# Kernel tuning notes

Measured on AMD Instinct MI355X. Metric: run time of the kernel, lower is better.

## Reference

```python
import jax, jax.numpy as jnp
import numpy as np

D_MODEL = 1024
NUM_HEADS = 16
D_K = D_MODEL // NUM_HEADS


def setup_inputs() -> dict:
    key = jax.random.key(0)
    ks = jax.random.split(key, 5)
    s = 1.0 / np.sqrt(D_MODEL)
    return {
        "x": jax.random.normal(ks[0], (2, 2048, D_MODEL), dtype=jnp.float32),
        "Wq": jax.random.normal(ks[1], (D_MODEL, D_MODEL), dtype=jnp.float32) * s,
        "bq": jnp.zeros((D_MODEL,), dtype=jnp.float32),
        "Wk": jax.random.normal(ks[2], (D_MODEL, D_MODEL), dtype=jnp.float32) * s,
        "bk": jnp.zeros((D_MODEL,), dtype=jnp.float32),
        "Wv": jax.random.normal(ks[3], (D_MODEL, D_MODEL), dtype=jnp.float32) * s,
        "bv": jnp.zeros((D_MODEL,), dtype=jnp.float32),
        "Wo": jax.random.normal(ks[4], (D_MODEL, D_MODEL), dtype=jnp.float32) * s,
        "bo": jnp.zeros((D_MODEL,), dtype=jnp.float32),
    }


def reference(x, Wq, bq, Wk, bk, Wv, bv, Wo, bo):
    B, S, D = x.shape
    H, dk = NUM_HEADS, D_K
    Q = x @ Wq + bq  # [B, S, D]
    K = x @ Wk + bk
    V = x @ Wv + bv
    # Faithful to the torch code: plain .view(B, H, S, dk) (NO transpose),
    # i.e. heads are carved out of the flattened (S*D) dim, not the feature dim.
    Q = Q.reshape(B, H, S, dk)
    K = K.reshape(B, H, S, dk)
    V = V.reshape(B, H, S, dk)
    scores = jnp.einsum("bhqd,bhkd->bhqk", Q, K) / jnp.sqrt(jnp.float32(dk))
    attn = jax.nn.softmax(scores, axis=-1)  # [B, H, S, S]
    ctx = jnp.einsum("bhqk,bhkd->bhqd", attn, V)  # [B, H, S, dk]
    out = ctx.reshape(B, S, D) @ Wo + bo
    return out  # dropout is identity in eval mode
```

## Files before the change

### kernel.cpp

```cpp
#include <hip/hip_runtime.h>
#include <hip/hip_bf16.h>
#include <math.h>

#define D_MODEL 1024
#define SEQ     2048
#define BATCH   2
#define NHEAD   16
#define DKH     64
#define BH      (BATCH * NHEAD)

typedef unsigned short u16;
typedef unsigned int   u32;
typedef __bf16 bf16x8 __attribute__((ext_vector_type(8)));
typedef float  f32x4  __attribute__((ext_vector_type(4)));

#define MFMA16(a, b, c) __builtin_amdgcn_mfma_f32_16x16x32_bf16((a), (b), (c), 0, 0, 0)
#define AS1 __attribute__((address_space(1)))
#define AS3 __attribute__((address_space(3)))

#define QSCALE 0.18033688f

__device__ __forceinline__ u16 f2bf(float x) {
    u32 u = __float_as_uint(x);
    u += 0x7fffu + ((u >> 16) & 1u);
    return (u16)(u >> 16);
}
__device__ __forceinline__ float bf2f(u16 b) {
    return __uint_as_float(((u32)b) << 16);
}
__device__ __forceinline__ void gl16(const u16* g, void* lds) {
    __builtin_amdgcn_global_load_lds((const AS1 u32*)g, (AS3 u32*)lds, 16, 0, 0);
}

__global__ __launch_bounds__(256) void conv_all(
    const float* __restrict__ x, u16* __restrict__ Xh, int n4,
    const float* __restrict__ W0, const float* __restrict__ W1,
    const float* __restrict__ W2, const float* __restrict__ W3,
    u16* __restrict__ H0, u16* __restrict__ L0, u16* __restrict__ H1, u16* __restrict__ L1,
    u16* __restrict__ H2, u16* __restrict__ L2, u16* __restrict__ H3, u16* __restrict__ L3)
{
    const int t = threadIdx.x;
    if ((int)blockIdx.x < 4096) {
        int i = blockIdx.x * 256 + t;
        if (i >= n4) return;
        float4 v = reinterpret_cast<const float4*>(x)[i];
        uint2 H;
        H.x = f2bf(v.x) | ((u32)f2bf(v.y) << 16);
        H.y = f2bf(v.z) | ((u32)f2bf(v.w) << 16);
        reinterpret_cast<uint2*>(Xh)[i] = H;
        return;
    }
    int id = blockIdx.x - 4096;
    int bx = id & 15, by = (id >> 4) & 15, bz = id >> 8;
    const float* W; u16 *Ht, *Lt;
    if (bz == 0)      { W = W0; Ht = H0; Lt = L0; }
    else if (bz == 1) { W = W1; Ht = H1; Lt = L1; }
    else if (bz == 2) { W = W2; Ht = H2; Lt = L2; }
    else              { W = W3; Ht = H3; Lt = L3; }

    __shared__ float T[64][65];
    const int n0 = bx * 64, k0 = by * 64;
    #pragma unroll
    for (int i = 0; i < 4; ++i) {
        int f = t + i * 256;
        int kr = f >> 4, ns = (f & 15) * 4;
        float4 v = *reinterpret_cast<const float4*>(&W[(size_t)(k0 + kr) * D_MODEL + n0 + ns]);
        T[kr][ns + 0] = v.x; T[kr][ns + 1] = v.y; T[kr][ns + 2] = v.z; T[kr][ns + 3] = v.w;
    }
    __syncthreads();
    #pragma unroll
    for (int i = 0; i < 4; ++i) {
        int f = t + i * 256;
        int nr = f >> 4, ks = (f & 15) * 4;
        u16 hh[4], ll[4];
        #pragma unroll
        for (int j = 0; j < 4; ++j) {
            float xv = T[ks + j][nr];
            u16 hb = f2bf(xv);
            hh[j] = hb;
            ll[j] = f2bf(xv - bf2f(hb));
        }
        uint2 H, L;
        H.x = hh[0] | ((u32)hh[1] << 16); H.y = hh[2] | ((u32)hh[3] << 16);
        L.x = ll[0] | ((u32)ll[1] << 16); L.y = ll[2] | ((u32)ll[3] << 16);
        size_t o = (size_t)(n0 + nr) * D_MODEL + k0 + ks;
        *reinterpret_cast<uint2*>(&Ht[o]) = H;
        *reinterpret_cast<uint2*>(&Lt[o]) = L;
    }
}

__global__ __launch_bounds__(512, 2) void gemm_qkv(
    const u16* __restrict__ AhG,
    const u16* __restrict__ Bqh, const u16* __restrict__ Bql,
    const u16* __restrict__ Bkh, const u16* __restrict__ Bkl,
    const u16* __restrict__ Bvh, const u16* __restrict__ Bvl,
    const float* __restrict__ bq, const float* __restrict__ bk, const float* __restrict__ bv,
    u16* __restrict__ Qb, u16* __restrict__ Kb, u16* __restrict__ Vb)
{
    constexpr int K = D_MODEL, N = D_MODEL;
    __shared__ u16 LB[2][28672];

    const int tid  = threadIdx.x;
    const int wv   = tid >> 6;
    const int lane = tid & 63;
    const int quad = lane >> 4;
    const int l16  = lane & 15;
    const int wm   = wv & 1, wn = wv >> 1;
    const int brow = blockIdx.y * 128, bcol = blockIdx.x * 128;

    const u16* sp[7];
    int sldb[7];
    #pragma unroll
    for (int j = 0; j < 7; ++j) {
        int c = (j < 3) ? (wv * 3 + j)
              : (j < 5) ? (24 + wv * 2 + (j - 3))
                        : (40 + wv * 2 + (j - 5));
        int a = c >> 3, cc = c & 7;
        int row = cc * 16 + (lane >> 2);
        int gseg = (lane & 3) ^ ((lane >> 3) & 3);
        const u16* p;
        if (a == 0)      p = AhG;
        else if (a == 1) p = Bqh;
        else if (a == 2) p = Bql;
        else if (a == 3) p = Bkh;
        else if (a == 4) p = Bkl;
        else if (a == 5) p = Bvh;
        else             p = Bvl;
        int rbase = (a == 0) ? brow : bcol;
        sp[j]   = p + (size_t)(rbase + row) * K + gseg * 8;
        sldb[j] = a * 8192 + cc * 1024;
    }

    int aro[4], bro[2];
    #pragma unroll
    for (int i = 0; i < 4; ++i) {
        int mr = wm * 64 + i * 16 + l16;
        aro[i] = mr * 64 + ((quad ^ ((mr >> 1) & 3)) * 16);
    }
    #pragma unroll
    for (int i = 0; i < 2; ++i) {
        int nr = wn * 32 + i * 16 + l16;
        bro[i] = nr * 64 + ((quad ^ ((nr >> 1) & 3)) * 16);
    }

    f32x4 acc[3][4][2] = {};

    auto rdB = [&](int cur, int m, bf16x8 (&bh)[2], bf16x8 (&bl)[2]) {
        const int bbh = (1 + 2 * m) * 8192, bbl = (2 + 2 * m) * 8192;
        #pragma unroll
        for (int i = 0; i < 2; ++i) {
            bh[i] = *reinterpret_cast<const bf16x8*>((const char*)LB[cur] + bbh + bro[i]);
            bl[i] = *reinterpret_cast<const bf16x8*>((const char*)LB[cur] + bbl + bro[i]);
        }
    };
    auto mm = [&](int m, bf16x8 (&ah)[4], bf16x8 (&bh)[2], bf16x8 (&bl)[2]) {
        __builtin_amdgcn_s_setprio(1);
        #pragma unroll
        for (int mi = 0; mi < 4; ++mi)
            #pragma unroll
            for (int ni = 0; ni < 2; ++ni) {
                f32x4 c = acc[m][mi][ni];
                c = MFMA16(ah[mi], bh[ni], c);
                c = MFMA16(ah[mi], bl[ni], c);
                acc[m][mi][ni] = c;
            }
        __builtin_amdgcn_s_setprio(0);
    };

    #pragma unroll
    for (int j = 0; j < 7; ++j)
        gl16(sp[j], (char*)LB[0] + sldb[j]);

    for (int it = 0; it < K / 32 - 1; ++it) {
        const int cur = it & 1, nx = cur ^ 1;
        const int k1 = (it + 1) * 32;
        bf16x8 ah[4], bh[2], bl[2];

        asm volatile("s_waitcnt vmcnt(4)" ::: "memory");
        __builtin_amdgcn_s_barrier();
        #pragma unroll
        for (int i = 0; i < 4; ++i)
            ah[i] = *reinterpret_cast<const bf16x8*>((const char*)LB[cur] + aro[i]);
        rdB(cur, 0, bh, bl);
        gl16(sp[0] + k1, (char*)LB[nx] + sldb[0]);
        gl16(sp[1] + k1, (char*)LB[nx] + sldb[1]);
        gl16(sp[2] + k1, (char*)LB[nx] + sldb[2]);
        mm(0, ah, bh, bl);

        asm volatile("s_waitcnt vmcnt(5)" ::: "memory");
        __builtin_amdgcn_s_barrier();
        rdB(cur, 1, bh, bl);
        gl16(sp[3] + k1, (char*)LB[nx] + sldb[3]);
        gl16(sp[4] + k1, (char*)LB[nx] + sldb[4]);
        mm(1, ah, bh, bl);

        asm volatile("s_waitcnt vmcnt(5)" ::: "memory");
        __builtin_amdgcn_s_barrier();
        rdB(cur, 2, bh, bl);
        gl16(sp[5] + k1, (char*)LB[nx] + sldb[5]);
        gl16(sp[6] + k1, (char*)LB[nx] + sldb[6]);
        mm(2, ah, bh, bl);
    }

    {
        const int cur = (K / 32 - 1) & 1;
        bf16x8 ah[4], bh[2], bl[2];

        asm volatile("s_waitcnt vmcnt(4)" ::: "memory");
        __builtin_amdgcn_s_barrier();
        #pragma unroll
        for (int i = 0; i < 4; ++i)
            ah[i] = *reinterpret_cast<const bf16x8*>((const char*)LB[cur] + aro[i]);
        rdB(cur, 0, bh, bl);
        mm(0, ah, bh, bl);

        asm volatile("s_waitcnt vmcnt(2)" ::: "memory");
        __builtin_amdgcn_s_barrier();
        rdB(cur, 1, bh, bl);
        mm(1, ah, bh, bl);

        asm volatile("s_waitcnt vmcnt(0)" ::: "memory");
        __builtin_amdgcn_s_barrier();
        rdB(cur, 2, bh, bl);
        mm(2, ah, bh, bl);
    }

    #pragma unroll
    for (int m = 0; m < 3; ++m) {
        const float* bias = (m == 0) ? bq : (m == 1) ? bk : bv;
        u16* out = (m == 0) ? Qb : (m == 1) ? Kb : Vb;
        const float sc = (m == 0) ? QSCALE : 1.0f;
        #pragma unroll
        for (int mi = 0; mi < 4; ++mi) {
            #pragma unroll
            for (int ni = 0; ni < 2; ++ni) {
                int col = bcol + wn * 32 + ni * 16 + l16;
                float bvv = bias[col];
                #pragma unroll
                for (int r = 0; r < 4; ++r) {
                    int row = brow + wm * 64 + mi * 16 + quad * 4 + r;
                    out[(size_t)row * N + col] = f2bf((acc[m][mi][ni][r] + bvv) * sc);
                }
            }
        }
    }
}

__global__ __launch_bounds__(512, 2) void gemm_oproj(
    const u16* __restrict__ AhG, const u16* __restrict__ Bh, const u16* __restrict__ Bl,
    const float* __restrict__ bias, float* __restrict__ Cf)
{
    constexpr int K = D_MODEL, N = D_MODEL;
    __shared__ u16 LB[2][12288];

    const int tid  = threadIdx.x;
    const int wv   = tid >> 6;
    const int lane = tid & 63;
    const int quad = lane >> 4;
    const int l16  = lane & 15;
    const int wm   = wv & 1, wn = wv >> 1;
    const int brow = blockIdx.y * 128, bcol = blockIdx.x * 128;

    const u16* sp[3];
    int sldb[3];
    #pragma unroll
    for (int j = 0; j < 3; ++j) {
        int c = wv * 3 + j, a = c >> 3, cc = c & 7;
        int row = cc * 16 + (lane >> 2);
        int gseg = (lane & 3) ^ ((lane >> 3) & 3);
        const u16* p = (a == 0) ? AhG : (a == 1) ? Bh : Bl;
        int rbase = (a == 0) ? brow : bcol;
        sp[j]   = p + (size_t)(rbase + row) * K + gseg * 8;
        sldb[j] = a * 8192 + cc * 1024;
    }

    int aro[4], bro[2];
    #pragma unroll
    for (int i = 0; i < 4; ++i) {
        int mr = wm * 64 + i * 16 + l16;
        aro[i] = mr * 64 + ((quad ^ ((mr >> 1) & 3)) * 16);
    }
    #pragma unroll
    for (int i = 0; i < 2; ++i) {
        int nr = wn * 32 + i * 16 + l16;
        bro[i] = nr * 64 + ((quad ^ ((nr >> 1) & 3)) * 16);
    }

    f32x4 acc[4][2] = {};

    #pragma unroll
    for (int j = 0; j < 3; ++j)
        gl16(sp[j], (char*)LB[0] + sldb[j]);

    for (int it = 0; it < K / 32; ++it) {
        const int cur = it & 1;
        __syncthreads();
        if (it + 1 < K / 32) {
            const int nxt = cur ^ 1;
            const int k1 = (it + 1) * 32;
            #pragma unroll
            for (int j = 0; j < 3; ++j)
                gl16(sp[j] + k1, (char*)LB[nxt] + sldb[j]);
        }

        bf16x8 ah[4], bh[2], bl[2];
        #pragma unroll
        for (int i = 0; i < 4; ++i)
            ah[i] = *reinterpret_cast<const bf16x8*>((const char*)LB[cur] + aro[i]);
        #pragma unroll
        for (int i = 0; i < 2; ++i) {
            bh[i] = *reinterpret_cast<const bf16x8*>((const char*)LB[cur] + 8192 + bro[i]);
            bl[i] = *reinterpret_cast<const bf16x8*>((const char*)LB[cur] + 16384 + bro[i]);
        }
        #pragma unroll
        for (int mi = 0; mi < 4; ++mi)
            #pragma unroll
            for (int ni = 0; ni < 2; ++ni) {
                f32x4 c = acc[mi][ni];
                c = MFMA16(ah[mi], bh[ni], c);
                c = MFMA16(ah[mi], bl[ni], c);
                acc[mi][ni] = c;
            }
    }

    #pragma unroll
    for (int mi = 0; mi < 4; ++mi) {
        #pragma unroll
        for (int ni = 0; ni < 2; ++ni) {
            int col = bcol + wn * 32 + ni * 16 + l16;
            float bvv = bias[col];
            #pragma unroll
            for (int r = 0; r < 4; ++r) {
                int row = brow + wm * 64 + mi * 16 + quad * 4 + r;
                Cf[(size_t)row * N + col] = acc[mi][ni][r] + bvv;
            }
        }
    }
}

__global__ __launch_bounds__(256) void v_transpose(
    const u16* __restrict__ V, u16* __restrict__ Vt)
{
    __shared__ u16 T[64][72];
    const int bh = blockIdx.y, st = blockIdx.x;
    const u16* src = V + ((size_t)bh * SEQ + (size_t)st * 64) * 64;
    const int t = threadIdx.x;
    #pragma unroll
    for (int i = 0; i < 2; ++i) {
        int c  = t + i * 256;
        int s  = c >> 3;
        int d0 = (c & 7) * 8;
        uint4 v = reinterpret_cast<const uint4*>(src)[c];
        u16 e[8];
        e[0] = (u16)(v.x & 0xffff); e[1] = (u16)(v.x >> 16);
        e[2] = (u16)(v.y & 0xffff); e[3] = (u16)(v.y >> 16);
        e[4] = (u16)(v.z & 0xffff); e[5] = (u16)(v.z >> 16);
        e[6] = (u16)(v.w & 0xffff); e[7] = (u16)(v.w >> 16);
        #pragma unroll
        for (int j = 0; j < 8; ++j) T[d0 + j][s] = e[j];
    }
    __syncthreads();
    const int d = t >> 2, seg = t & 3;
    u16* dst = Vt + (size_t)bh * 64 * SEQ + (size_t)d * SEQ + st * 64;
    #pragma unroll
    for (int gg = 0; gg < 2; ++gg) {
        int g = seg * 2 + gg;
        u32 r0 = *reinterpret_cast<const u32*>(&T[d][2 * g]);
        u32 r1 = *reinterpret_cast<const u32*>(&T[d][2 * g + 16]);
        u32 r2 = *reinterpret_cast<const u32*>(&T[d][2 * g + 32]);
        u32 r3 = *reinterpret_cast<const u32*>(&T[d][2 * g + 48]);
        uint4 w;
        w.x = (r0 & 0xffffu) | (r1 << 16);
        w.y = (r2 & 0xffffu) | (r3 << 16);
        w.z = (r0 >> 16) | (r1 & 0xffff0000u);
        w.w = (r2 >> 16) | (r3 & 0xffff0000u);
        *reinterpret_cast<uint4*>(&dst[8 * g]) = w;
    }
}

__global__ __launch_bounds__(512, 4) void attn_mfma(
    const u16* __restrict__ Qb_g, const u16* __restrict__ Kb_g,
    const u16* __restrict__ Vt_g, u16* __restrict__ Ch_g)
{
    __shared__ u16 KVS[3][8192];
    __shared__ u16 Pb [128 * 72];

    const int tid  = threadIdx.x;
    const int wv   = tid >> 6;
    const int lane = tid & 63;
    const int quad = lane >> 4;
    const int l16  = lane & 15;
    const int id   = blockIdx.x;
    const int bh   = id & 31;
    const int qt   = id >> 5;
    const int qrow = wv * 16;

    const size_t qbase = ((size_t)bh * SEQ + (size_t)qt * 128) * 64;
    const size_t kbh   = (size_t)bh * SEQ * 64;
    const size_t vtbh  = (size_t)bh * 64 * SEQ;

    bf16x8 qf[2];
    #pragma unroll
    for (int ks = 0; ks < 2; ++ks) {
        size_t o = qbase + (size_t)(qrow + l16) * 64 + ks * 32 + quad * 8;
        qf[ks] = *reinterpret_cast<const bf16x8*>(Qb_g + o);
    }

    const u16* sp[2];
    size_t sstep[2];
    int sldb[2];
    #pragma unroll
    for (int j = 0; j < 2; ++j) {
        int c   = wv * 2 + j;
        int arr = c >> 3, cc = c & 7;
        int row = cc * 8 + (lane >> 3);
        int sg  = (lane & 7) ^ (row & 7);
        if (arr == 0) { sp[j] = Kb_g + kbh + (size_t)row * 64 + sg * 8;   sstep[j] = 4096; }
        else          { sp[j] = Vt_g + vtbh + (size_t)row * SEQ + sg * 8; sstep[j] = 64; }
        sldb[j] = arr * 8192 + cc * 1024;
    }

    int fro[4][2];
    #pragma unroll
    for (int t = 0; t < 4; ++t)
        #pragma unroll
        for (int ks = 0; ks < 2; ++ks)
            fro[t][ks] = (t * 16 + l16) * 128 + (((ks * 4 + quad) ^ (l16 & 7)) * 16);

    bf16x8 onesv;
    #pragma unroll
    for (int i = 0; i < 8; ++i) onesv[i] = (__bf16)1.0f;

    f32x4 oacc[4] = {};
    f32x4 lsum = {};

    auto S_step = [&](int bufidx, f32x4 (&sacc)[4]) {
        const char* kb = (const char*)KVS[bufidx];
        #pragma unroll
        for (int t4 = 0; t4 < 4; ++t4) {
            bf16x8 kh0 = *reinterpret_cast<const bf16x8*>(kb + fro[t4][0]);
            bf16x8 kh1 = *reinterpret_cast<const bf16x8*>(kb + fro[t4][1]);
            f32x4 a = sacc[t4];
            a = MFMA16(qf[0], kh0, a);
            a = MFMA16(qf[1], kh1, a);
            sacc[t4] = a;
        }
    };

    auto PV_step = [&](int bufidx) {
        const char* vb = (const char*)KVS[bufidx] + 8192;
        bf16x8 bvf[4][2];
        #pragma unroll
        for (int dt = 0; dt < 4; ++dt) {
            bvf[dt][0] = *reinterpret_cast<const bf16x8*>(vb + fro[dt][0]);
            bvf[dt][1] = *reinterpret_cast<const bf16x8*>(vb + fro[dt][1]);
        }
        bf16x8 ap[2];
        #pragma unroll
        for (int ks = 0; ks < 2; ++ks)
            ap[ks] = *reinterpret_cast<const bf16x8*>(
                &Pb[(qrow + l16) * 72 + ks * 32 + quad * 8]);
        #pragma unroll
        for (int dt = 0; dt < 4; ++dt) {
            oacc[dt] = MFMA16(ap[0], bvf[dt][0], oacc[dt]);
            oacc[dt] = MFMA16(ap[1], bvf[dt][1], oacc[dt]);
        }
        lsum = MFMA16(ap[0], onesv, lsum);
        lsum = MFMA16(ap[1], onesv, lsum);
    };

    auto EXP2_step = [&](f32x4 (&sacc)[4]) {
        const int rowb = qrow + quad * 4;
        #pragma unroll
        for (int r = 0; r < 4; ++r) {
            u32 u0 = __float_as_uint(__builtin_amdgcn_exp2f(sacc[0][r]));
            u32 u1 = __float_as_uint(__builtin_amdgcn_exp2f(sacc[1][r]));
            u32 u2 = __float_as_uint(__builtin_amdgcn_exp2f(sacc[2][r]));
            u32 u3 = __float_as_uint(__builtin_amdgcn_exp2f(sacc[3][r]));
            uint2 w;
            w.x = (u0 >> 16) | (u1 & 0xffff0000u);
            w.y = (u2 >> 16) | (u3 & 0xffff0000u);
            *reinterpret_cast<uint2*>(&Pb[(rowb + r) * 72 + l16 * 4]) = w;
        }
    };

    #pragma unroll
    for (int j = 0; j < 2; ++j)
        gl16(sp[j], (char*)KVS[0] + sldb[j]);

    {
        __syncthreads();
        #pragma unroll
        for (int j = 0; j < 2; ++j)
            gl16(sp[j] + sstep[j], (char*)KVS[1] + sldb[j]);
        f32x4 sacc[4] = {};
        __builtin_amdgcn_s_setprio(1);
        S_step(0, sacc);
        __builtin_amdgcn_s_setprio(0);
        EXP2_step(sacc);
    }

    int cur = 1, prv = 0, nxt = 2;
    for (int kt = 1; kt < SEQ / 64; ++kt) {
        __syncthreads();
        if (kt + 1 < SEQ / 64) {
            #pragma unroll
            for (int j = 0; j < 2; ++j)
                gl16(sp[j] + (size_t)(kt + 1) * sstep[j], (char*)KVS[nxt] + sldb[j]);
        }

        f32x4 sacc[4] = {};
        __builtin_amdgcn_s_setprio(1);
        S_step(cur, sacc);
        PV_step(prv);
        __builtin_amdgcn_s_setprio(0);
        EXP2_step(sacc);

        prv = cur; cur = nxt; nxt = (nxt == 2) ? 0 : nxt + 1;
    }

    __builtin_amdgcn_s_setprio(1);
    PV_step(prv);
    __builtin_amdgcn_s_setprio(0);

    u16* Oh = Ch_g + qbase;
    float inv[4];
    #pragma unroll
    for (int r = 0; r < 4; ++r) inv[r] = 1.0f / lsum[r];
    #pragma unroll
    for (int dt = 0; dt < 4; ++dt)
        #pragma unroll
        for (int r = 0; r < 4; ++r) {
            int row = qrow + quad * 4 + r;
            Oh[(size_t)row * 64 + dt * 16 + l16] = f2bf(oacc[dt][r] * inv[r]);
        }
}

extern "C" void kernel_launch(void* const* d_in, const int* in_sizes, int n_in,
                              void* d_out, int out_size, void* d_ws, size_t ws_size,
                              hipStream_t stream)
{
    const float* x  = (const float*)d_in[0];
    const float* Wq = (const float*)d_in[1];
    const float* bq = (const float*)d_in[2];
    const float* Wk = (const float*)d_in[3];
    const float* bk = (const float*)d_in[4];
    const float* Wv = (const float*)d_in[5];
    const float* bv = (const float*)d_in[6];
    const float* Wo = (const float*)d_in[7];
    const float* bo = (const float*)d_in[8];
    float* out = (float*)d_out;

    const int M = BATCH * SEQ;
    const int N = D_MODEL;
    const size_t NE = (size_t)M * N;
    const size_t NW = (size_t)N * N;

    u16* w16 = (u16*)d_ws;
    u16* Xh   = w16;
    u16* Qb   = Xh   + NE;
    u16* Kb   = Qb   + NE;
    u16* Vb   = Kb   + NE;
    u16* Vtb  = Vb   + NE;
    u16* Ctxh = Vtb  + NE;
    u16* WTqh = Ctxh + NE;
    u16* WTql = WTqh + NW;
    u16* WTkh = WTql + NW;
    u16* WTkl = WTkh + NW;
    u16* WTvh = WTkl + NW;
    u16* WTvl = WTvh + NW;
    u16* WToh = WTvl + NW;
    u16* WTol = WToh + NW;

    conv_all<<<dim3(4096 + 1024), dim3(256), 0, stream>>>(
        x, Xh, (int)(NE / 4),
        Wq, Wk, Wv, Wo, WTqh, WTql, WTkh, WTkl, WTvh, WTvl, WToh, WTol);

    gemm_qkv<<<dim3(N / 128, M / 128), dim3(512), 0, stream>>>(
        Xh, WTqh, WTql, WTkh, WTkl, WTvh, WTvl, bq, bk, bv, Qb, Kb, Vb);

    v_transpose<<<dim3(SEQ / 64, BH), dim3(256), 0, stream>>>(Vb, Vtb);

    attn_mfma<<<dim3((SEQ / 128) * BH), dim3(512), 0, stream>>>(Qb, Kb, Vtb, Ctxh);

    gemm_oproj<<<dim3(N / 128, M / 128), dim3(512), 0, stream>>>(
        Ctxh, WToh, WTol, bo, out);
}
```

Baseline: 211.9 us.

## Load low-part weight fragments directly from global into registers, bypassing LDS

```diff
diff --git a/kernel.cpp b/kernel.cpp
--- a/kernel.cpp
+++ b/kernel.cpp
@@ -98,7 +98,7 @@
     u16* __restrict__ Qb, u16* __restrict__ Kb, u16* __restrict__ Vb)
 {
     constexpr int K = D_MODEL, N = D_MODEL;
-    __shared__ u16 LB[2][28672];
+    __shared__ u16 LB[2][16384];
 
     const int tid  = threadIdx.x;
     const int wv   = tid >> 6;
@@ -108,27 +108,18 @@
     const int wm   = wv & 1, wn = wv >> 1;
     const int brow = blockIdx.y * 128, bcol = blockIdx.x * 128;
 
-    const u16* sp[7];
-    int sldb[7];
-    #pragma unroll
-    for (int j = 0; j < 7; ++j) {
-        int c = (j < 3) ? (wv * 3 + j)
-              : (j < 5) ? (24 + wv * 2 + (j - 3))
-                        : (40 + wv * 2 + (j - 5));
-        int a = c >> 3, cc = c & 7;
-        int row = cc * 16 + (lane >> 2);
+    const u16* sp[4];
+    int sldb[4];
+    {
+        int row  = wv * 16 + (lane >> 2);
         int gseg = (lane & 3) ^ ((lane >> 3) & 3);
-        const u16* p;
-        if (a == 0)      p = AhG;
-        else if (a == 1) p = Bqh;
-        else if (a == 2) p = Bql;
-        else if (a == 3) p = Bkh;
-        else if (a == 4) p = Bkl;
-        else if (a == 5) p = Bvh;
-        else             p = Bvl;
-        int rbase = (a == 0) ? brow : bcol;
-        sp[j]   = p + (size_t)(rbase + row) * K + gseg * 8;
-        sldb[j] = a * 8192 + cc * 1024;
+        const u16* ps[4] = { AhG, Bqh, Bkh, Bvh };
+        #pragma unroll
+        for (int j = 0; j < 4; ++j) {
+            int rbase = (j == 0) ? brow : bcol;
+            sp[j]   = ps[j] + (size_t)(rbase + row) * K + gseg * 8;
+            sldb[j] = j * 8192 + wv * 1024;
+        }
     }
 
     int aro[4], bro[2];
@@ -143,86 +134,103 @@
         bro[i] = nr * 64 + ((quad ^ ((nr >> 1) & 3)) * 16);
     }
 
+    const int r0 = bcol + wn * 32 + l16, r1 = r0 + 16;
+    const int qo = quad * 8;
+
     f32x4 acc[3][4][2] = {};
 
-    auto rdB = [&](int cur, int m, bf16x8 (&bh)[2], bf16x8 (&bl)[2]) {
-        const int bbh = (1 + 2 * m) * 8192, bbl = (2 + 2 * m) * 8192;
-        #pragma unroll
-        for (int i = 0; i < 2; ++i) {
-            bh[i] = *reinterpret_cast<const bf16x8*>((const char*)LB[cur] + bbh + bro[i]);
-            bl[i] = *reinterpret_cast<const bf16x8*>((const char*)LB[cur] + bbl + bro[i]);
-        }
-    };
-    auto mm = [&](int m, bf16x8 (&ah)[4], bf16x8 (&bh)[2], bf16x8 (&bl)[2]) {
+    auto mm2 = [&](int m, bf16x8 (&ah)[4], bf16x8 bh0, bf16x8 bh1,
+                   bf16x8 bl0, bf16x8 bl1) {
         __builtin_amdgcn_s_setprio(1);
         #pragma unroll
-        for (int mi = 0; mi < 4; ++mi)
-            #pragma unroll
-            for (int ni = 0; ni < 2; ++ni) {
-                f32x4 c = acc[m][mi][ni];
-                c = MFMA16(ah[mi], bh[ni], c);
-                c = MFMA16(ah[mi], bl[ni], c);
-                acc[m][mi][ni] = c;
-            }
+        for (int mi = 0; mi < 4; ++mi) {
+            f32x4 c0 = acc[m][mi][0], c1 = acc[m][mi][1];
+            c0 = MFMA16(ah[mi], bh0, c0);
+            c1 = MFMA16(ah[mi], bh1, c1);
+            c0 = MFMA16(ah[mi], bl0, c0);
+            c1 = MFMA16(ah[mi], bl1, c1);
+            acc[m][mi][0] = c0; acc[m][mi][1] = c1;
+        }
         __builtin_amdgcn_s_setprio(0);
     };
 
     #pragma unroll
-    for (int j = 0; j < 7; ++j)
+    for (int j = 0; j < 4; ++j)
         gl16(sp[j], (char*)LB[0] + sldb[j]);
+    bf16x8 pql0 = *reinterpret_cast<const bf16x8*>(Bql + (size_t)r0 * K + qo);
+    bf16x8 pql1 = *reinterpret_cast<const bf16x8*>(Bql + (size_t)r1 * K + qo);
 
     for (int it = 0; it < K / 32 - 1; ++it) {
         const int cur = it & 1, nx = cur ^ 1;
         const int k1 = (it + 1) * 32;
-        bf16x8 ah[4], bh[2], bl[2];
-
-        asm volatile("s_waitcnt vmcnt(4)" ::: "memory");
+        const int kk = it * 32 + qo;
+
+        bf16x8 kl0 = *reinterpret_cast<const bf16x8*>(Bkl + (size_t)r0 * K + kk);
+        bf16x8 kl1 = *reinterpret_cast<const bf16x8*>(Bkl + (size_t)r1 * K + kk);
+        bf16x8 vl0 = *reinterpret_cast<const bf16x8*>(Bvl + (size_t)r0 * K + kk);
+        bf16x8 vl1 = *reinterpret_cast<const bf16x8*>(Bvl + (size_t)r1 * K + kk);
+
+        asm volatile("s_waitcnt vmcnt(6)" ::: "memory");
         __builtin_amdgcn_s_barrier();
+
+        gl16(sp[0] + k1, (char*)LB[nx] + sldb[0]);
+        gl16(sp[1] + k1, (char*)LB[nx] + sldb[1]);
+        bf16x8 ah[4];
         #pragma unroll
         for (int i = 0; i < 4; ++i)
             ah[i] = *reinterpret_cast<const bf16x8*>((const char*)LB[cur] + aro[i]);
-        rdB(cur, 0, bh, bl);
-        gl16(sp[0] + k1, (char*)LB[nx] + sldb[0]);
-        gl16(sp[1] + k1, (char*)LB[nx] + sldb[1]);
+        bf16x8 bh0 = *reinterpret_cast<const bf16x8*>((const char*)LB[cur] + 8192 + bro[0]);
+        bf16x8 bh1 = *reinterpret_cast<const bf16x8*>((const char*)LB[cur] + 8192 + bro[1]);
+        asm volatile("s_waitcnt vmcnt(6)" ::: "memory");
+        mm2(0, ah, bh0, bh1, pql0, pql1);
+
         gl16(sp[2] + k1, (char*)LB[nx] + sldb[2]);
-        mm(0, ah, bh, bl);
-
+        bh0 = *reinterpret_cast<const bf16x8*>((const char*)LB[cur] + 16384 + bro[0]);
+        bh1 = *reinterpret_cast<const bf16x8*>((const char*)LB[cur] + 16384 + bro[1]);
         asm volatile("s_waitcnt vmcnt(5)" ::: "memory");
+        mm2(1, ah, bh0, bh1, kl0, kl1);
+
+        gl16(sp[3] + k1, (char*)LB[nx] + sldb[3]);
+        bh0 = *reinterpret_cast<const bf16x8*>((const char*)LB[cur] + 24576 + bro[0]);
+        bh1 = *reinterpret_cast<const bf16x8*>((const char*)LB[cur] + 24576 + bro[1]);
+        asm volatile("s_waitcnt vmcnt(4)" ::: "memory");
+        mm2(2, ah, bh0, bh1, vl0, vl1);
+
+        pql0 = *reinterpret_cast<const bf16x8*>(Bql + (size_t)r0 * K + k1 + qo);
+        pql1 = *reinterpret_cast<const bf16x8*>(Bql + (size_t)r1 * K + k1 + qo);
+    }
+
+    {
+        const int it = K / 32 - 1;
+        const int cur = it & 1;
+        const int kk = it * 32 + qo;
+
+        bf16x8 kl0 = *reinterpret_cast<const bf16x8*>(Bkl + (size_t)r0 * K + kk);
+        bf16x8 kl1 = *reinterpret_cast<const bf16x8*>(Bkl + (size_t)r1 * K + kk);
+        bf16x8 vl0 = *reinterpret_cast<const bf16x8*>(Bvl + (size_t)r0 * K + kk);
+        bf16x8 vl1 = *reinterpret_cast<const bf16x8*>(Bvl + (size_t)r1 * K + kk);
+
+        asm volatile("s_waitcnt vmcnt(6)" ::: "memory");
         __builtin_amdgcn_s_barrier();
-        rdB(cur, 1, bh, bl);
-        gl16(sp[3] + k1, (char*)LB[nx] + sldb[3]);
-        gl16(sp[4] + k1, (char*)LB[nx] + sldb[4]);
-        mm(1, ah, bh, bl);
-
-        asm volatile("s_waitcnt vmcnt(5)" ::: "memory");
-        __builtin_amdgcn_s_barrier();
-        rdB(cur, 2, bh, bl);
-        gl16(sp[5] + k1, (char*)LB[nx] + sldb[5]);
-        gl16(sp[6] + k1, (char*)LB[nx] + sldb[6]);
-        mm(2, ah, bh, bl);
-    }
-
-    {
-        const int cur = (K / 32 - 1) & 1;
-        bf16x8 ah[4], bh[2], bl[2];
-
-        asm volatile("s_waitcnt vmcnt(4)" ::: "memory");
-        __builtin_amdgcn_s_barrier();
+
+        bf16x8 ah[4];
         #pragma unroll
         for (int i = 0; i < 4; ++i)
             ah[i] = *reinterpret_cast<const bf16x8*>((const char*)LB[cur] + aro[i]);
-        rdB(cur, 0, bh, bl);
-        mm(0, ah, bh, bl);
-
+        bf16x8 bh0 = *reinterpret_cast<const bf16x8*>((const char*)LB[cur] + 8192 + bro[0]);
+        bf16x8 bh1 = *reinterpret_cast<const bf16x8*>((const char*)LB[cur] + 8192 + bro[1]);
+        asm volatile("s_waitcnt vmcnt(4)" ::: "memory");
+        mm2(0, ah, bh0, bh1, pql0, pql1);
+
+        bh0 = *reinterpret_cast<const bf16x8*>((const char*)LB[cur] + 16384 + bro[0]);
+        bh1 = *reinterpret_cast<const bf16x8*>((const char*)LB[cur] + 16384 + bro[1]);
         asm volatile("s_waitcnt vmcnt(2)" ::: "memory");
-        __builtin_amdgcn_s_barrier();
-        rdB(cur, 1, bh, bl);
-        mm(1, ah, bh, bl);
-
+        mm2(1, ah, bh0, bh1, kl0, kl1);
+
+        bh0 = *reinterpret_cast<const bf16x8*>((const char*)LB[cur] + 24576 + bro[0]);
+        bh1 = *reinterpret_cast<const bf16x8*>((const char*)LB[cur] + 24576 + bro[1]);
         asm volatile("s_waitcnt vmcnt(0)" ::: "memory");
-        __builtin_amdgcn_s_barrier();
-        rdB(cur, 2, bh, bl);
-        mm(2, ah, bh, bl);
+        mm2(2, ah, bh0, bh1, vl0, vl1);
     }
 
     #pragma unroll
@@ -251,7 +259,7 @@
     const float* __restrict__ bias, float* __restrict__ Cf)
 {
     constexpr int K = D_MODEL, N = D_MODEL;
-    __shared__ u16 LB[2][12288];
+    __shared__ u16 LB[2][8192];
 
     const int tid  = threadIdx.x;
     const int wv   = tid >> 6;
@@ -261,17 +269,15 @@
     const int wm   = wv & 1, wn = wv >> 1;
     const int brow = blockIdx.y * 128, bcol = blockIdx.x * 128;
 
-    const u16* sp[3];
-    int sldb[3];
-    #pragma unroll
-    for (int j = 0; j < 3; ++j) {
-        int c = wv * 3 + j, a = c >> 3, cc = c & 7;
-        int row = cc * 16 + (lane >> 2);
+    const u16* sp[2];
+    int sldb[2];
+    {
+        int row  = wv * 16 + (lane >> 2);
         int gseg = (lane & 3) ^ ((lane >> 3) & 3);
-        const u16* p = (a == 0) ? AhG : (a == 1) ? Bh : Bl;
-        int rbase = (a == 0) ? brow : bcol;
-        sp[j]   = p + (size_t)(rbase + row) * K + gseg * 8;
-        sldb[j] = a * 8192 + cc * 1024;
+        sp[0]   = AhG + (size_t)(brow + row) * K + gseg * 8;
+        sp[1]   = Bh  + (size_t)(bcol + row) * K + gseg * 8;
+        sldb[0] = wv * 1024;
+        sldb[1] = 8192 + wv * 1024;
     }
 
     int aro[4], bro[2];
@@ -286,41 +292,72 @@
         bro[i] = nr * 64 + ((quad ^ ((nr >> 1) & 3)) * 16);
     }
 
+    const int r0 = bcol + wn * 32 + l16, r1 = r0 + 16;
+    const int qo = quad * 8;
+
     f32x4 acc[4][2] = {};
 
-    #pragma unroll
-    for (int j = 0; j < 3; ++j)
-        gl16(sp[j], (char*)LB[0] + sldb[j]);
-
-    for (int it = 0; it < K / 32; ++it) {
-        const int cur = it & 1;
-        __syncthreads();
-        if (it + 1 < K / 32) {
-            const int nxt = cur ^ 1;
-            const int k1 = (it + 1) * 32;
-            #pragma unroll
-            for (int j = 0; j < 3; ++j)
-                gl16(sp[j] + k1, (char*)LB[nxt] + sldb[j]);
-        }
-
-        bf16x8 ah[4], bh[2], bl[2];
+    gl16(sp[0], (char*)LB[0] + sldb[0]);
+    gl16(sp[1], (char*)LB[0] + sldb[1]);
+    bf16x8 pbl0 = *reinterpret_cast<const bf16x8*>(Bl + (size_t)r0 * K + qo);
+    bf16x8 pbl1 = *reinterpret_cast<const bf16x8*>(Bl + (size_t)r1 * K + qo);
+
+    for (int it = 0; it < K / 32 - 1; ++it) {
+        const int cur = it & 1, nx = cur ^ 1;
+        const int k1 = (it + 1) * 32;
+
+        asm volatile("s_waitcnt vmcnt(2)" ::: "memory");
+        __builtin_amdgcn_s_barrier();
+
+        gl16(sp[0] + k1, (char*)LB[nx] + sldb[0]);
+        gl16(sp[1] + k1, (char*)LB[nx] + sldb[1]);
+
+        bf16x8 ah[4], bh0, bh1;
         #pragma unroll
         for (int i = 0; i < 4; ++i)
             ah[i] = *reinterpret_cast<const bf16x8*>((const char*)LB[cur] + aro[i]);
-        #pragma unroll
-        for (int i = 0; i < 2; ++i) {
-            bh[i] = *reinterpret_cast<const bf16x8*>((const char*)LB[cur] + 8192 + bro[i]);
-            bl[i] = *reinterpret_cast<const bf16x8*>((const char*)LB[cur] + 16384 + bro[i]);
-        }
-        #pragma unroll
-        for (int mi = 0; mi < 4; ++mi)
-            #pragma unroll
-            for (int ni = 0; ni < 2; ++ni) {
-                f32x4 c = acc[mi][ni];
-                c = MFMA16(ah[mi], bh[ni], c);
-                c = MFMA16(ah[mi], bl[ni], c);
-                acc[mi][ni] = c;
-            }
+        bh0 = *reinterpret_cast<const bf16x8*>((const char*)LB[cur] + 8192 + bro[0]);
+        bh1 = *reinterpret_cast<const bf16x8*>((const char*)LB[cur] + 8192 + bro[1]);
+
+        asm volatile("s_waitcnt vmcnt(2)" ::: "memory");
+        __builtin_amdgcn_s_setprio(1);
+        #pragma unroll
+        for (int mi = 0; mi < 4; ++mi) {
+            f32x4 c0 = acc[mi][0], c1 = acc[mi][1];
+            c0 = MFMA16(ah[mi], bh0, c0);
+            c1 = MFMA16(ah[mi], bh1, c1);
+            c0 = MFMA16(ah[mi], pbl0, c0);
+            c1 = MFMA16(ah[mi], pbl1, c1);
+            acc[mi][0] = c0; acc[mi][1] = c1;
+        }
+        __builtin_amdgcn_s_setprio(0);
+
+        pbl0 = *reinterpret_cast<const bf16x8*>(Bl + (size_t)r0 * K + k1 + qo);
+        pbl1 = *reinterpret_cast<const bf16x8*>(Bl + (size_t)r1 * K + k1 + qo);
+    }
+
+    {
+        const int cur = (K / 32 - 1) & 1;
+        asm volatile("s_waitcnt vmcnt(2)" ::: "memory");
+        __builtin_amdgcn_s_barrier();
+        bf16x8 ah[4], bh0, bh1;
+        #pragma unroll
+        for (int i = 0; i < 4; ++i)
+            ah[i] = *reinterpret_cast<const bf16x8*>((const char*)LB[cur] + aro[i]);
+        bh0 = *reinterpret_cast<const bf16x8*>((const char*)LB[cur] + 8192 + bro[0]);
+        bh1 = *reinterpret_cast<const bf16x8*>((const char*)LB[cur] + 8192 + bro[1]);
+        asm volatile("s_waitcnt vmcnt(0)" ::: "memory");
+        __builtin_amdgcn_s_setprio(1);
+        #pragma unroll
+        for (int mi = 0; mi < 4; ++mi) {
+            f32x4 c0 = acc[mi][0], c1 = acc[mi][1];
+            c0 = MFMA16(ah[mi], bh0, c0);
+            c1 = MFMA16(ah[mi], bh1, c1);
+            c0 = MFMA16(ah[mi], pbl0, c0);
+            c1 = MFMA16(ah[mi], pbl1, c1);
+            acc[mi][0] = c0; acc[mi][1] = c1;
+        }
+        __builtin_amdgcn_s_setprio(0);
     }
 
     #pragma unroll
```

Measured after the change: 234.7 us. 1.11x slower.

## Split O-projection GEMM K-step into two phases with fine-grained vmcnt waits

Applied to the files above, without the earlier changes.

```diff
diff --git a/kernel.cpp b/kernel.cpp
--- a/kernel.cpp
+++ b/kernel.cpp
@@ -263,15 +263,15 @@
 
     const u16* sp[3];
     int sldb[3];
-    #pragma unroll
-    for (int j = 0; j < 3; ++j) {
-        int c = wv * 3 + j, a = c >> 3, cc = c & 7;
-        int row = cc * 16 + (lane >> 2);
+    {
+        int row  = wv * 16 + (lane >> 2);
         int gseg = (lane & 3) ^ ((lane >> 3) & 3);
-        const u16* p = (a == 0) ? AhG : (a == 1) ? Bh : Bl;
-        int rbase = (a == 0) ? brow : bcol;
-        sp[j]   = p + (size_t)(rbase + row) * K + gseg * 8;
-        sldb[j] = a * 8192 + cc * 1024;
+        sp[0]   = AhG + (size_t)(brow + row) * K + gseg * 8;
+        sp[1]   = Bh  + (size_t)(bcol + row) * K + gseg * 8;
+        sp[2]   = Bl  + (size_t)(bcol + row) * K + gseg * 8;
+        sldb[0] = wv * 1024;
+        sldb[1] = 8192 + wv * 1024;
+        sldb[2] = 16384 + wv * 1024;
     }
 
     int aro[4], bro[2];
@@ -288,39 +288,64 @@
 
     f32x4 acc[4][2] = {};
 
+    auto mmc = [&](bf16x8 (&ah)[4], bf16x8 b0, bf16x8 b1) {
+        __builtin_amdgcn_s_setprio(1);
+        #pragma unroll
+        for (int mi = 0; mi < 4; ++mi) {
+            f32x4 c0 = acc[mi][0], c1 = acc[mi][1];
+            c0 = MFMA16(ah[mi], b0, c0);
+            c1 = MFMA16(ah[mi], b1, c1);
+            acc[mi][0] = c0; acc[mi][1] = c1;
+        }
+        __builtin_amdgcn_s_setprio(0);
+    };
+
     #pragma unroll
     for (int j = 0; j < 3; ++j)
         gl16(sp[j], (char*)LB[0] + sldb[j]);
 
-    for (int it = 0; it < K / 32; ++it) {
-        const int cur = it & 1;
-        __syncthreads();
-        if (it + 1 < K / 32) {
-            const int nxt = cur ^ 1;
-            const int k1 = (it + 1) * 32;
-            #pragma unroll
-            for (int j = 0; j < 3; ++j)
-                gl16(sp[j] + k1, (char*)LB[nxt] + sldb[j]);
-        }
-
-        bf16x8 ah[4], bh[2], bl[2];
+    for (int it = 0; it < K / 32 - 1; ++it) {
+        const int cur = it & 1, nx = cur ^ 1;
+        const int k1 = (it + 1) * 32;
+        bf16x8 ah[4], b0, b1;
+
+        asm volatile("s_waitcnt vmcnt(1)" ::: "memory");
+        __builtin_amdgcn_s_barrier();
         #pragma unroll
         for (int i = 0; i < 4; ++i)
             ah[i] = *reinterpret_cast<const bf16x8*>((const char*)LB[cur] + aro[i]);
-        #pragma unroll
-        for (int i = 0; i < 2; ++i) {
-            bh[i] = *reinterpret_cast<const bf16x8*>((const char*)LB[cur] + 8192 + bro[i]);
-            bl[i] = *reinterpret_cast<const bf16x8*>((const char*)LB[cur] + 16384 + bro[i]);
-        }
-        #pragma unroll
-        for (int mi = 0; mi < 4; ++mi)
-            #pragma unroll
-            for (int ni = 0; ni < 2; ++ni) {
-                f32x4 c = acc[mi][ni];
-                c = MFMA16(ah[mi], bh[ni], c);
-                c = MFMA16(ah[mi], bl[ni], c);
-                acc[mi][ni] = c;
-            }
+        b0 = *reinterpret_cast<const bf16x8*>((const char*)LB[cur] + 8192 + bro[0]);
+        b1 = *reinterpret_cast<const bf16x8*>((const char*)LB[cur] + 8192 + bro[1]);
+        gl16(sp[0] + k1, (char*)LB[nx] + sldb[0]);
+        gl16(sp[1] + k1, (char*)LB[nx] + sldb[1]);
+        mmc(ah, b0, b1);
+
+        asm volatile("s_waitcnt vmcnt(2)" ::: "memory");
+        __builtin_amdgcn_s_barrier();
+        b0 = *reinterpret_cast<const bf16x8*>((const char*)LB[cur] + 16384 + bro[0]);
+        b1 = *reinterpret_cast<const bf16x8*>((const char*)LB[cur] + 16384 + bro[1]);
+        gl16(sp[2] + k1, (char*)LB[nx] + sldb[2]);
+        mmc(ah, b0, b1);
+    }
+
+    {
+        const int cur = (K / 32 - 1) & 1;
+        bf16x8 ah[4], b0, b1;
+
+        asm volatile("s_waitcnt vmcnt(1)" ::: "memory");
+        __builtin_amdgcn_s_barrier();
+        #pragma unroll
+        for (int i = 0; i < 4; ++i)
+            ah[i] = *reinterpret_cast<const bf16x8*>((const char*)LB[cur] + aro[i]);
+        b0 = *reinterpret_cast<const bf16x8*>((const char*)LB[cur] + 8192 + bro[0]);
+        b1 = *reinterpret_cast<const bf16x8*>((const char*)LB[cur] + 8192 + bro[1]);
+        mmc(ah, b0, b1);
+
+        asm volatile("s_waitcnt vmcnt(0)" ::: "memory");
+        __builtin_amdgcn_s_barrier();
+        b0 = *reinterpret_cast<const bf16x8*>((const char*)LB[cur] + 16384 + bro[0]);
+        b1 = *reinterpret_cast<const bf16x8*>((const char*)LB[cur] + 16384 + bro[1]);
+        mmc(ah, b0, b1);
     }
 
     #pragma unroll
```

Result: no change. 208.6 us (-1.6%).
